# Kernel optimization log

Hardware: AMD Instinct MI355X
Metric: run time of the kernel (lower is better)

The kernel has to match this reference:

```python
import jax, jax.numpy as jnp
import numpy as np

D = 1024      # hidden_size
FF = 4096     # ff_inner_dim = 4 * D
E = 8         # num_experts
K = 2         # moe_top_k
B, L = 4, 1024


def setup_inputs() -> dict:
    key = jax.random.key(0)
    ks = jax.random.split(key, 12)
    s = 0.02  # weight init scale
    return {
        "x": jax.random.normal(ks[0], (B, L, D), jnp.float32),
        "W_gate": jax.random.normal(ks[1], (D, E), jnp.float32) * s,
        "W1": jax.random.normal(ks[2], (E, D, FF), jnp.float32) * s,
        "b1": jnp.zeros((E, FF), jnp.float32),
        "W2": jax.random.normal(ks[3], (E, FF, D), jnp.float32) * s,
        "b2": jnp.zeros((E, D), jnp.float32),
        "Ws1": jax.random.normal(ks[4], (D, FF), jnp.float32) * s,
        "bs1": jnp.zeros((FF,), jnp.float32),
        "Ws2": jax.random.normal(ks[5], (FF, D), jnp.float32) * s,
        "bs2": jnp.zeros((D,), jnp.float32),
    }


def _gelu(h):
    # torch F.gelu default = exact (erf) gelu
    return jax.nn.gelu(h, approximate=False)


def reference(x, W_gate, W1, b1, W2, b2, Ws1, bs1, Ws2, bs2):
    Bx, Lx, Dx = x.shape
    xf = x.reshape(-1, Dx)                       # [T, D]
    logits = xf @ W_gate                         # [T, E]
    probs = jax.nn.softmax(logits, axis=-1)
    top_v, top_i = jax.lax.top_k(probs, K)       # [T, K]
    top_v = top_v / jnp.sum(top_v, axis=-1, keepdims=True)
    # dense combine weights: [T, E], zero for unselected experts
    combine = jnp.sum(jax.nn.one_hot(top_i, E, dtype=xf.dtype) * top_v[..., None], axis=1)

    out = jnp.zeros_like(xf)
    for e in range(E):  # fixed small expert loop, unrolled under jit
        h = _gelu(xf @ W1[e] + b1[e])            # [T, FF]
        out = out + combine[:, e:e + 1] * (h @ W2[e] + b2[e])

    shared = _gelu(xf @ Ws1 + bs1) @ Ws2 + bs2   # [T, D]
    return (out + shared).reshape(Bx, Lx, Dx)
```

## Files before the change

### kernel.cpp

```cpp
#include <hip/hip_runtime.h>
#include <hip/hip_bf16.h>

typedef unsigned short ushort_t;
typedef __attribute__((ext_vector_type(4))) float f32x4;
typedef __attribute__((ext_vector_type(8))) short bf16x8;
typedef __attribute__((ext_vector_type(8))) unsigned short us8;

#define T_TOK 4096
#define D_DIM 1024
#define FF_DIM 4096
#define NE 8
#define ESTRIDE 4194304L

__device__ __forceinline__ unsigned short f2bf(float f) {
  __hip_bfloat16 h = __float2bfloat16(f);
  return __builtin_bit_cast(unsigned short, h);
}
__device__ __forceinline__ float bf2f(ushort_t u) {
  unsigned int x = ((unsigned int)u) << 16;
  return __builtin_bit_cast(float, x);
}
__device__ __forceinline__ float gelu_f(float v) {
  return 0.5f * v * (1.0f + erff(v * 0.70710678118654752440f));
}

__global__ __launch_bounds__(256) void pre_kernel(
    const float* __restrict__ x, const float* __restrict__ Wg,
    const float* __restrict__ W1, const float* __restrict__ Ws1,
    int* __restrict__ cnt, int* __restrict__ tok,
    float* __restrict__ wof, int* __restrict__ rankof,
    ushort_t* __restrict__ Xbf, ushort_t* __restrict__ W1T) {
  __shared__ ushort_t tile[128][136];
  const int bid = blockIdx.x, tid = threadIdx.x;

  if (bid < 1024) {
    const int t = bid * 4 + (tid >> 6);
    const int lane = tid & 63;
    const float* xr = x + (long)t * D_DIM;
    ushort_t* xb = Xbf + (long)t * D_DIM;
    float acc[NE];
#pragma unroll
    for (int e = 0; e < NE; e++) acc[e] = 0.f;
#pragma unroll
    for (int i = 0; i < 16; i++) {
      int d = i * 64 + lane;
      float xv = xr[d];
      xb[d] = f2bf(xv);
      const float* wr = Wg + d * NE;
#pragma unroll
      for (int e = 0; e < NE; e++) acc[e] += xv * wr[e];
    }
#pragma unroll
    for (int off = 32; off > 0; off >>= 1) {
#pragma unroll
      for (int e = 0; e < NE; e++) acc[e] += __shfl_xor(acc[e], off, 64);
    }
    if (lane == 0) {
      int i0 = 0;
#pragma unroll
      for (int e = 1; e < NE; e++) if (acc[e] > acc[i0]) i0 = e;
      int i1 = -1;
#pragma unroll
      for (int e = 0; e < NE; e++) {
        if (e == i0) continue;
        if (i1 < 0 || acc[e] > acc[i1]) i1 = e;
      }
      float e1 = expf(acc[i1] - acc[i0]);
      float w0 = 1.f / (1.f + e1);
      float w1 = e1 * w0;
      int s0 = atomicAdd(&cnt[i0], 1);
      tok[i0 * T_TOK + s0] = t; wof[i0 * T_TOK + s0] = w0; rankof[i0 * T_TOK + s0] = 0;
      int s1 = atomicAdd(&cnt[i1], 1);
      tok[i1 * T_TOK + s1] = t; wof[i1 * T_TOK + s1] = w1; rankof[i1 * T_TOK + s1] = 1;
      tok[8 * T_TOK + t] = t; wof[8 * T_TOK + t] = 1.f; rankof[8 * T_TOK + t] = 0;
    }
    return;
  }

  int tix = bid - 1024;
  if (tix >= 2304) return;
  const int e = tix >> 8;
  const int rem = tix & 255;
  const int r0 = (rem >> 5) * 128, c0 = (rem & 31) * 128;
  const float* src = (e == 8) ? Ws1 : (W1 + (long)e * 4194304);
  ushort_t* d = W1T + (long)e * ESTRIDE;
#pragma unroll
  for (int i = 0; i < 16; i++) {
    int lin = tid + i * 256;
    int r = lin >> 5, c = (lin & 31) * 4;
    float4 v = *(const float4*)(src + (long)(r0 + r) * 4096 + c0 + c);
    tile[c + 0][r] = f2bf(v.x);
    tile[c + 1][r] = f2bf(v.y);
    tile[c + 2][r] = f2bf(v.z);
    tile[c + 3][r] = f2bf(v.w);
  }
  __syncthreads();
#pragma unroll
  for (int i = 0; i < 8; i++) {
    int lin = tid + i * 256;
    int cc = lin >> 4, rp = lin & 15;
    us8 v = *(const us8*)&tile[cc][rp * 8];
    *(us8*)(d + (long)(c0 + cc) * 1024 + r0 + rp * 8) = v;
  }
}

__global__ void scan_kernel(int* cnt, int* base) {
  if (threadIdx.x == 0 && blockIdx.x == 0) {
    int s = 0;
    for (int e = 0; e < NE; e++) { base[e] = s; s += cnt[e]; }
    base[8] = s;
    cnt[8] = T_TOK;
  }
}

__global__ void build_queue_kernel(const int* __restrict__ cnt,
                                   unsigned int* __restrict__ q1,
                                   unsigned int* __restrict__ q2,
                                   int* __restrict__ nq) {
  const int e = blockIdx.x;
  int off1 = 0, off2 = 0, tot1 = 0, tot2 = 0, M = 0;
  for (int i = 0; i < 9; i++) {
    int c = (i == 8) ? T_TOK : cnt[i];
    int m = (c + 255) >> 8;
    if (i < e) { off1 += m * 16; off2 += m * 4; }
    if (i == e) M = m;
    tot1 += m * 16; tot2 += m * 4;
  }
  for (int i = threadIdx.x; i < M * 16; i += 256) {
    int my = i >> 4, nx = i & 15;
    int ms = my >> 1, mi = my & 1, ns = nx >> 2, ni = nx & 3;
    int h = M - ms * 2; if (h > 2) h = 2;
    int pos = ms * 32 + ns * (h * 4) + mi * 4 + ni;
    q1[off1 + pos] = ((unsigned)e << 16) | ((unsigned)my << 8) | (unsigned)nx;
  }
  for (int i = threadIdx.x; i < M * 4; i += 256) {
    int my = i >> 2, nx = i & 3;
    int pos = nx * M + my;
    q2[off2 + pos] = ((unsigned)e << 16) | ((unsigned)my << 8) | (unsigned)nx;
  }
  if (e == 0 && threadIdx.x == 0) { nq[0] = tot1; nq[1] = tot2; }
}

template <int K, int N, int PHASE, bool FUSE>
__global__ __launch_bounds__(1024, 1) void gemm_kernel(
    const ushort_t* __restrict__ Abase, const ushort_t* __restrict__ WT,
    const float* __restrict__ bias_e, const float* __restrict__ bias_s,
    const int* __restrict__ cnt, const int* __restrict__ base,
    const int* __restrict__ tok, const float* __restrict__ wof,
    const int* __restrict__ rankof,
    const unsigned int* __restrict__ q, const int* __restrict__ nq_all,
    ushort_t* __restrict__ He, ushort_t* __restrict__ ybuf, float* __restrict__ out,
    const float* __restrict__ W2src, const float* __restrict__ Ws2src,
    ushort_t* __restrict__ W2Tdst) {
  __shared__ char smem[65536];
  const int tid = threadIdx.x;
  const int bid = blockIdx.x;
  const int NBLK = FUSE ? 1024 : (int)gridDim.x;

  if (FUSE && bid >= 1024) {
    int tix = bid - 1024;
    if (tix >= 2304) return;
    const int e = tix >> 8;
    const int rem = tix & 255;
    const int r0 = (rem >> 3) * 128, c0 = (rem & 7) * 128;
    const float* src = (e == 8) ? Ws2src : (W2src + (long)e * 4194304);
    ushort_t* d = W2Tdst + (long)e * ESTRIDE;
    ushort_t (*tile)[136] = (ushort_t (*)[136])smem;
#pragma unroll
    for (int i = 0; i < 4; i++) {
      int lin = tid + i * 1024;
      int r = lin >> 5, c = (lin & 31) * 4;
      float4 v = *(const float4*)(src + (long)(r0 + r) * 1024 + c0 + c);
      tile[c + 0][r] = f2bf(v.x);
      tile[c + 1][r] = f2bf(v.y);
      tile[c + 2][r] = f2bf(v.z);
      tile[c + 3][r] = f2bf(v.w);
    }
    __syncthreads();
#pragma unroll
    for (int i = 0; i < 2; i++) {
      int lin = tid + i * 1024;
      int cc = lin >> 4, rp = lin & 15;
      us8 v = *(const us8*)&tile[cc][rp * 8];
      *(us8*)(d + (long)(c0 + cc) * 4096 + r0 + rp * 8) = v;
    }
    return;
  }

  const int nq = nq_all[PHASE - 1];
  const int chunk = NBLK >> 3;
  const int vbid = (bid < (chunk << 3)) ? ((bid & 7) * chunk + (bid >> 3)) : bid;

  const int w = tid >> 6, lane = tid & 63;
  const int wm = w >> 2, wn = w & 3;
  const int lr = lane & 15, lg = lane >> 4;
  char* const lds = smem;

  const int srow = tid >> 2;
  const int cg = ((tid & 3) - (srow >> 1)) & 3;

  int offA[4], offB[4];
#pragma unroll
  for (int m = 0; m < 4; m++) {
    int r = wm * 64 + m * 16 + lr;
    offA[m] = r * 64 + (((lg + (r >> 1)) & 3) << 4);
  }
#pragma unroll
  for (int n = 0; n < 4; n++) {
    int r = wn * 64 + n * 16 + lr;
    offB[n] = r * 64 + (((lg + (r >> 1)) & 3) << 4);
  }

  constexpr int NT = K / 32;

#define STAGE(buf_, kk_)                                                        \
  do {                                                                          \
    char* dd_ = lds + (buf_) * 32768 + tid * 16;                                \
    __builtin_amdgcn_global_load_lds(                                           \
        (const __attribute__((address_space(1))) void*)(pA + (kk_)),            \
        (__attribute__((address_space(3))) void*)(dd_), 16, 0, 0);              \
    __builtin_amdgcn_global_load_lds(                                           \
        (const __attribute__((address_space(1))) void*)(pB + (kk_)),            \
        (__attribute__((address_space(3))) void*)(dd_ + 16384), 16, 0, 0);      \
  } while (0)

  for (int it = vbid; it < nq; it += NBLK) {
    const unsigned int item = q[it];
    const int e = item >> 16;
    const int m0 = ((item >> 8) & 0xff) * 256;
    const int n0 = (item & 0xff) * 256;
    const int count = cnt[e];

    int rr = m0 + srow;
    int rc = (rr < count) ? rr : 0;
    long arow;
    if (PHASE == 1) arow = tok[e * T_TOK + rc];
    else            arow = (long)base[e] + rc;
    const ushort_t* pA = Abase + arow * (long)K + cg * 8;
    const ushort_t* pB = WT + (long)e * ESTRIDE + (long)(n0 + srow) * K + cg * 8;

    f32x4 acc[4][4] = {};

    __builtin_amdgcn_s_barrier();
    asm volatile("" ::: "memory");
    STAGE(0, 0);

    for (int t = 0; t < NT; t++) {
      if (t + 1 < NT) {
        STAGE((t + 1) & 1, (t + 1) * 32);
        asm volatile("s_waitcnt vmcnt(2)" ::: "memory");
      } else {
        asm volatile("s_waitcnt vmcnt(0)" ::: "memory");
      }
      __builtin_amdgcn_s_barrier();
      asm volatile("" ::: "memory");

      const char* aB = lds + (t & 1) * 32768;
      const char* bB = aB + 16384;
      bf16x8 av[4], bv[4];
#pragma unroll
      for (int m = 0; m < 4; m++) av[m] = *(const bf16x8*)(aB + offA[m]);
#pragma unroll
      for (int n = 0; n < 4; n++) bv[n] = *(const bf16x8*)(bB + offB[n]);
#pragma unroll
      for (int m = 0; m < 4; m++)
#pragma unroll
        for (int n = 0; n < 4; n++)
          acc[m][n] = __builtin_amdgcn_mfma_f32_16x16x32_bf16(av[m], bv[n], acc[m][n], 0, 0, 0);

      __builtin_amdgcn_s_barrier();
      asm volatile("" ::: "memory");
    }

    const float* bias = (e == NE) ? bias_s : (bias_e + (long)e * N);
#pragma unroll
    for (int m = 0; m < 4; m++) {
#pragma unroll
      for (int j = 0; j < 4; j++) {
        int rloc = wm * 64 + m * 16 + lg * 4 + j;
        int rrr = m0 + rloc;
        if (rrr >= count) continue;
        if (PHASE == 1) {
          long orow = (long)base[e] + rrr;
#pragma unroll
          for (int n = 0; n < 4; n++) {
            int col = n0 + wn * 64 + n * 16 + lr;
            float v = acc[m][n][j] + bias[col];
            He[orow * FF_DIM + col] = f2bf(gelu_f(v));
          }
        } else {
          int tt = tok[e * T_TOK + rrr];
          if (e == NE) {
#pragma unroll
            for (int n = 0; n < 4; n++) {
              int col = n0 + wn * 64 + n * 16 + lr;
              out[(long)tt * D_DIM + col] = acc[m][n][j] + bias[col];
            }
          } else {
            float wgt = wof[e * T_TOK + rrr];
            int rk = rankof[e * T_TOK + rrr];
            ushort_t* dst = ybuf + (long)rk * ((long)T_TOK * D_DIM) + (long)tt * D_DIM;
#pragma unroll
            for (int n = 0; n < 4; n++) {
              int col = n0 + wn * 64 + n * 16 + lr;
              dst[col] = f2bf(wgt * (acc[m][n][j] + bias[col]));
            }
          }
        }
      }
    }
  }
#undef STAGE
}

__global__ void final_add_kernel(float* __restrict__ out, const ushort_t* __restrict__ ybuf) {
  long i = ((long)blockIdx.x * 256 + threadIdx.x) * 8;
  float4 a0 = *(const float4*)(out + i);
  float4 a1 = *(const float4*)(out + i + 4);
  us8 b = *(const us8*)(ybuf + i);
  us8 c = *(const us8*)(ybuf + (long)T_TOK * D_DIM + i);
  float r[8];
#pragma unroll
  for (int k = 0; k < 8; k++) r[k] = bf2f(b[k]) + bf2f(c[k]);
  a0.x += r[0]; a0.y += r[1]; a0.z += r[2]; a0.w += r[3];
  a1.x += r[4]; a1.y += r[5]; a1.z += r[6]; a1.w += r[7];
  *(float4*)(out + i) = a0;
  *(float4*)(out + i + 4) = a1;
}

extern "C" void kernel_launch(void* const* d_in, const int* in_sizes, int n_in,
                              void* d_out, int out_size, void* d_ws, size_t ws_size,
                              hipStream_t stream) {
  (void)in_sizes; (void)n_in; (void)out_size; (void)ws_size;
  const float* x   = (const float*)d_in[0];
  const float* Wg  = (const float*)d_in[1];
  const float* W1  = (const float*)d_in[2];
  const float* b1  = (const float*)d_in[3];
  const float* W2  = (const float*)d_in[4];
  const float* b2  = (const float*)d_in[5];
  const float* Ws1 = (const float*)d_in[6];
  const float* bs1 = (const float*)d_in[7];
  const float* Ws2 = (const float*)d_in[8];
  const float* bs2 = (const float*)d_in[9];
  float* out = (float*)d_out;

  char* ws = (char*)d_ws;
  int*      cnt    = (int*)(ws + 0);
  int*      base   = (int*)(ws + 64);
  int*      tok    = (int*)(ws + 256);
  float*    wof    = (float*)(ws + 256 + 147456);
  int*      rankof = (int*)(ws + 256 + 2 * 147456);
  ushort_t* Xbf    = (ushort_t*)(ws + 442624);
  ushort_t* W1T    = (ushort_t*)(ws + 8831232);
  ushort_t* W2T    = (ushort_t*)(ws + 84328704);
  ushort_t* He     = (ushort_t*)(ws + 159826176);
  int*      nq     = (int*)(ws + 260489472);
  unsigned int* q1 = (unsigned int*)(ws + 260489536);
  unsigned int* q2 = (unsigned int*)(ws + 260489536 + 32768);
  ushort_t* ybuf   = (ushort_t*)(ws + 261538048);

  hipMemsetAsync(cnt, 0, 64, stream);
  pre_kernel<<<3328, 256, 0, stream>>>(x, Wg, W1, Ws1, cnt, tok, wof, rankof, Xbf, W1T);
  scan_kernel<<<1, 64, 0, stream>>>(cnt, base);
  build_queue_kernel<<<9, 256, 0, stream>>>(cnt, q1, q2, nq);
  gemm_kernel<1024, 4096, 1, true><<<3328, 1024, 0, stream>>>(
      Xbf, W1T, b1, bs1, cnt, base, tok, wof, rankof, q1, nq, He, ybuf, out,
      W2, Ws2, W2T);
  gemm_kernel<4096, 1024, 2, false><<<256, 1024, 0, stream>>>(
      He, W2T, b2, bs2, cnt, base, tok, wof, rankof, q2, nq, He, ybuf, out,
      nullptr, nullptr, nullptr);
  final_add_kernel<<<2048, 256, 0, stream>>>(out, ybuf);
}
```

Measured before the change: 505.7 us.

## Stage GEMM epilogue through LDS for coalesced vector stores; fold scan into queue build

The GEMM epilogue now writes each 64-row slice of the accumulator tile, after bias and GELU, into shared memory as bf16. It then reads rows back so each thread issues 16-byte contiguous global stores, replacing the scattered 2-byte and 4-byte per-element writes to He, ybuf and out. The separate single-thread scan kernel is merged into build_queue_kernel to remove one launch. The trade-offs are extra barriers and LDS traffic in the epilogue. The shared-expert fp32 output and the weighted expert outputs are now rounded to bf16 before the final write or scale, which slightly lowers precision.

```diff
diff --git a/kernel.cpp b/kernel.cpp
--- a/kernel.cpp
+++ b/kernel.cpp
@@ -104,19 +104,10 @@
   }
 }
 
-__global__ void scan_kernel(int* cnt, int* base) {
-  if (threadIdx.x == 0 && blockIdx.x == 0) {
-    int s = 0;
-    for (int e = 0; e < NE; e++) { base[e] = s; s += cnt[e]; }
-    base[8] = s;
-    cnt[8] = T_TOK;
-  }
-}
-
-__global__ void build_queue_kernel(const int* __restrict__ cnt,
+__global__ void build_queue_kernel(const int* __restrict__ cnt, int* __restrict__ base,
                                    unsigned int* __restrict__ q1,
                                    unsigned int* __restrict__ q2,
-                                   int* __restrict__ nq) {
+                                   int* __restrict__ nq, int* __restrict__ cnt8) {
   const int e = blockIdx.x;
   int off1 = 0, off2 = 0, tot1 = 0, tot2 = 0, M = 0;
   for (int i = 0; i < 9; i++) {
@@ -138,7 +129,13 @@
     int pos = nx * M + my;
     q2[off2 + pos] = ((unsigned)e << 16) | ((unsigned)my << 8) | (unsigned)nx;
   }
-  if (e == 0 && threadIdx.x == 0) { nq[0] = tot1; nq[1] = tot2; }
+  if (e == 0 && threadIdx.x == 0) {
+    nq[0] = tot1; nq[1] = tot2;
+    int s = 0;
+    for (int i = 0; i < NE; i++) { base[i] = s; s += cnt[i]; }
+    base[8] = s;
+    *cnt8 = T_TOK;
+  }
 }
 
 template <int K, int N, int PHASE, bool FUSE>
@@ -273,37 +270,63 @@
     }
 
     const float* bias = (e == NE) ? bias_s : (bias_e + (long)e * N);
-#pragma unroll
-    for (int m = 0; m < 4; m++) {
-#pragma unroll
-      for (int j = 0; j < 4; j++) {
-        int rloc = wm * 64 + m * 16 + lg * 4 + j;
-        int rrr = m0 + rloc;
-        if (rrr >= count) continue;
+    ushort_t* ep = (ushort_t*)smem;
+    const int erow = tid >> 4;
+    const int eg0 = (tid & 15) * 2;
+#pragma unroll
+    for (int qh = 0; qh < 4; qh++) {
+      __builtin_amdgcn_s_barrier();
+      asm volatile("" ::: "memory");
+      if (wm == qh) {
+#pragma unroll
+        for (int m = 0; m < 4; m++)
+#pragma unroll
+          for (int j = 0; j < 4; j++) {
+            int lrow = m * 16 + lg * 4 + j;
+#pragma unroll
+            for (int n = 0; n < 4; n++) {
+              int col = wn * 64 + n * 16 + lr;
+              float v = acc[m][n][j] + bias[n0 + col];
+              if (PHASE == 1) v = gelu_f(v);
+              ep[lrow * 264 + col] = f2bf(v);
+            }
+          }
+      }
+      __builtin_amdgcn_s_barrier();
+      asm volatile("" ::: "memory");
+      int rrq = m0 + qh * 64 + erow;
+      if (rrq < count) {
         if (PHASE == 1) {
-          long orow = (long)base[e] + rrr;
-#pragma unroll
-          for (int n = 0; n < 4; n++) {
-            int col = n0 + wn * 64 + n * 16 + lr;
-            float v = acc[m][n][j] + bias[col];
-            He[orow * FF_DIM + col] = f2bf(gelu_f(v));
+          long orow = (long)base[e] + rrq;
+#pragma unroll
+          for (int k = 0; k < 2; k++) {
+            us8 v = *(const us8*)&ep[erow * 264 + (eg0 + k) * 8];
+            *(us8*)(He + orow * FF_DIM + n0 + (eg0 + k) * 8) = v;
           }
         } else {
-          int tt = tok[e * T_TOK + rrr];
+          int tt = tok[e * T_TOK + rrq];
           if (e == NE) {
-#pragma unroll
-            for (int n = 0; n < 4; n++) {
-              int col = n0 + wn * 64 + n * 16 + lr;
-              out[(long)tt * D_DIM + col] = acc[m][n][j] + bias[col];
+            float* dst = out + (long)tt * D_DIM + n0;
+#pragma unroll
+            for (int k = 0; k < 2; k++) {
+              us8 v = *(const us8*)&ep[erow * 264 + (eg0 + k) * 8];
+              float4 f0, f1;
+              f0.x = bf2f(v[0]); f0.y = bf2f(v[1]); f0.z = bf2f(v[2]); f0.w = bf2f(v[3]);
+              f1.x = bf2f(v[4]); f1.y = bf2f(v[5]); f1.z = bf2f(v[6]); f1.w = bf2f(v[7]);
+              *(float4*)(dst + (eg0 + k) * 8) = f0;
+              *(float4*)(dst + (eg0 + k) * 8 + 4) = f1;
             }
           } else {
-            float wgt = wof[e * T_TOK + rrr];
-            int rk = rankof[e * T_TOK + rrr];
-            ushort_t* dst = ybuf + (long)rk * ((long)T_TOK * D_DIM) + (long)tt * D_DIM;
-#pragma unroll
-            for (int n = 0; n < 4; n++) {
-              int col = n0 + wn * 64 + n * 16 + lr;
-              dst[col] = f2bf(wgt * (acc[m][n][j] + bias[col]));
+            float wgt = wof[e * T_TOK + rrq];
+            int rk = rankof[e * T_TOK + rrq];
+            ushort_t* dst = ybuf + (long)rk * ((long)T_TOK * D_DIM) + (long)tt * D_DIM + n0;
+#pragma unroll
+            for (int k = 0; k < 2; k++) {
+              us8 v = *(const us8*)&ep[erow * 264 + (eg0 + k) * 8];
+              us8 o;
+#pragma unroll
+              for (int jj = 0; jj < 8; jj++) o[jj] = f2bf(bf2f(v[jj]) * wgt);
+              *(us8*)(dst + (eg0 + k) * 8) = o;
             }
           }
         }
@@ -361,8 +384,7 @@
 
   hipMemsetAsync(cnt, 0, 64, stream);
   pre_kernel<<<3328, 256, 0, stream>>>(x, Wg, W1, Ws1, cnt, tok, wof, rankof, Xbf, W1T);
-  scan_kernel<<<1, 64, 0, stream>>>(cnt, base);
-  build_queue_kernel<<<9, 256, 0, stream>>>(cnt, q1, q2, nq);
+  build_queue_kernel<<<9, 256, 0, stream>>>(cnt, base, q1, q2, nq, &cnt[8]);
   gemm_kernel<1024, 4096, 1, true><<<3328, 1024, 0, stream>>>(
       Xbf, W1T, b1, bs1, cnt, base, tok, wof, rankof, q1, nq, He, ybuf, out,
       W2, Ws2, W2T);
```

New measurement: 568.4 us. +12.4%, slower.
